# Kernel optimization log

Hardware: AMD Instinct MI355X
Metric: run time of the kernel (lower is better)

The kernel has to match this reference:

```python
import jax, jax.numpy as jnp
import numpy as np

N = 50000      # nodes
E = 800000     # edges (avg degree 16)
D = 64         # dim_inner
L = 2          # layers_mp
OUT = 2        # dim_out (fraud / not fraud)
LN_EPS = 1e-5


def setup_inputs() -> dict:
    key = jax.random.key(0)
    ks = jax.random.split(key, 12)
    rn = lambda k, shape: jax.random.normal(k, shape, dtype=jnp.float32) * 0.05
    return {
        "x": jax.random.normal(ks[0], (N, D), dtype=jnp.float32),
        "edge_attr": jax.random.normal(ks[1], (E, D), dtype=jnp.float32),
        "edge_index": jax.random.randint(ks[2], (2, E), 0, N),
        # GINEConv inner MLP: Linear(D,D) -> ReLU -> Linear(D,D), stacked over L layers
        "gine_w1": rn(ks[3], (L, D, D)), "gine_b1": jnp.zeros((L, D), jnp.float32),
        "gine_w2": rn(ks[4], (L, D, D)), "gine_b2": jnp.zeros((L, D), jnp.float32),
        # edge-update MLP: Linear(3D,D) -> ReLU -> Linear(D,D)
        "em_w1": rn(ks[5], (L, 3 * D, D)), "em_b1": jnp.zeros((L, D), jnp.float32),
        "em_w2": rn(ks[6], (L, D, D)), "em_b2": jnp.zeros((L, D), jnp.float32),
        # per-layer LayerNorm params
        "ln_g": jnp.ones((L, D), jnp.float32), "ln_b": jnp.zeros((L, D), jnp.float32),
        # post_mp head: Linear(D, OUT)
        "head_w": rn(ks[7], (D, OUT)), "head_b": jnp.zeros((OUT,), jnp.float32),
    }


def _layernorm(h, g, b):
    mu = h.mean(axis=-1, keepdims=True)
    var = h.var(axis=-1, keepdims=True)
    return (h - mu) * jax.lax.rsqrt(var + LN_EPS) * g + b


def reference(x, edge_attr, edge_index, gine_w1, gine_b1, gine_w2, gine_b2,
              em_w1, em_b1, em_w2, em_b2, ln_g, ln_b, head_w, head_b):
    src, dst = edge_index[0], edge_index[1]
    e = edge_attr
    for i in range(L):
        # GINEConv: sum_{j->i} relu(x_j + e_ji), eps=0 so (1+eps)*x_i = x_i
        msg = jax.nn.relu(x[src] + e)                         # [E, D] gather + fuse
        agg = jax.ops.segment_sum(msg, dst, num_segments=N)   # [N, D] scatter-add
        h = x + agg
        h = jax.nn.relu(h @ gine_w1[i] + gine_b1[i]) @ gine_w2[i] + gine_b2[i]
        # norm -> activation (dropout p=0 in eval)
        x = jax.nn.relu(_layernorm(h, ln_g[i], ln_b[i]))
        # edge update: e = e + emlp(cat[x_src, x_dst, e]) / 2
        cat = jnp.concatenate([x[src], x[dst], e], axis=-1)   # [E, 3D]
        e = e + (jax.nn.relu(cat @ em_w1[i] + em_b1[i]) @ em_w2[i] + em_b2[i]) * 0.5
    # post_mp head on node features
    return x @ head_w + head_b
```

## Files before the change

### kernel.cpp

```cpp
#include <hip/hip_runtime.h>
#include <hip/hip_bf16.h>

#define NN 50000
#define NE 800000
#define D 64
#define K3 (3 * D)
#define LNEPS 1e-5f
#define STR 68
#define SINB 200
#define SHB 72
#define SEB 68

typedef __attribute__((ext_vector_type(8))) short bf16x8;
typedef __attribute__((ext_vector_type(4))) float f32x4;

__device__ __forceinline__ unsigned cvt2(float lo, float hi) {
  __hip_bfloat162 h = __float22bfloat162_rn(make_float2(lo, hi));
  return *(unsigned*)&h;
}
__device__ __forceinline__ unsigned short f2bf(float f) {
  __hip_bfloat16 h = __float2bfloat16(f);
  return *(unsigned short*)&h;
}
__device__ __forceinline__ float bf2f(unsigned short s) {
  return __uint_as_float((unsigned)s << 16);
}

#define FMA4x4(v, w)                                                  \
  a0.x = fmaf(v.x, w.x, a0.x); a0.y = fmaf(v.x, w.y, a0.y);           \
  a0.z = fmaf(v.x, w.z, a0.z); a0.w = fmaf(v.x, w.w, a0.w);           \
  a1.x = fmaf(v.y, w.x, a1.x); a1.y = fmaf(v.y, w.y, a1.y);           \
  a1.z = fmaf(v.y, w.z, a1.z); a1.w = fmaf(v.y, w.w, a1.w);           \
  a2.x = fmaf(v.z, w.x, a2.x); a2.y = fmaf(v.z, w.y, a2.y);           \
  a2.z = fmaf(v.z, w.z, a2.z); a2.w = fmaf(v.z, w.w, a2.w);           \
  a3.x = fmaf(v.w, w.x, a3.x); a3.y = fmaf(v.w, w.y, a3.y);           \
  a3.z = fmaf(v.w, w.z, a3.z); a3.w = fmaf(v.w, w.w, a3.w);

#define FMA2x4(v, w)                                                  \
  a0.x = fmaf(v.x, w.x, a0.x); a0.y = fmaf(v.x, w.y, a0.y);           \
  a0.z = fmaf(v.x, w.z, a0.z); a0.w = fmaf(v.x, w.w, a0.w);           \
  a1.x = fmaf(v.y, w.x, a1.x); a1.y = fmaf(v.y, w.y, a1.y);           \
  a1.z = fmaf(v.y, w.z, a1.z); a1.w = fmaf(v.y, w.w, a1.w);

#define HSTORE_RELU(buf)                                              \
  buf[(j0+0)*STR + t0+0] = fmaxf(a0.x, 0.f);                          \
  buf[(j0+1)*STR + t0+0] = fmaxf(a0.y, 0.f);                          \
  buf[(j0+2)*STR + t0+0] = fmaxf(a0.z, 0.f);                          \
  buf[(j0+3)*STR + t0+0] = fmaxf(a0.w, 0.f);                          \
  buf[(j0+0)*STR + t0+1] = fmaxf(a1.x, 0.f);                          \
  buf[(j0+1)*STR + t0+1] = fmaxf(a1.y, 0.f);                          \
  buf[(j0+2)*STR + t0+1] = fmaxf(a1.z, 0.f);                          \
  buf[(j0+3)*STR + t0+1] = fmaxf(a1.w, 0.f);                          \
  buf[(j0+0)*STR + t0+2] = fmaxf(a2.x, 0.f);                          \
  buf[(j0+1)*STR + t0+2] = fmaxf(a2.y, 0.f);                          \
  buf[(j0+2)*STR + t0+2] = fmaxf(a2.z, 0.f);                          \
  buf[(j0+3)*STR + t0+2] = fmaxf(a2.w, 0.f);                          \
  buf[(j0+0)*STR + t0+3] = fmaxf(a3.x, 0.f);                          \
  buf[(j0+1)*STR + t0+3] = fmaxf(a3.y, 0.f);                          \
  buf[(j0+2)*STR + t0+3] = fmaxf(a3.z, 0.f);                          \
  buf[(j0+3)*STR + t0+3] = fmaxf(a3.w, 0.f);

__global__ __launch_bounds__(256) void count_kernel(
    const int* __restrict__ dst, int* __restrict__ deg) {
  int e = blockIdx.x * 256 + threadIdx.x;
  if (e < NE) atomicAdd(&deg[dst[e]], 1);
}

__global__ __launch_bounds__(1024) void scan_reduce_kernel(
    const int* __restrict__ deg, int* __restrict__ bsum) {
  __shared__ int sS[16];
  int i = blockIdx.x * 1024 + threadIdx.x;
  int v = (i < NN) ? deg[i] : 0;
#pragma unroll
  for (int o = 32; o > 0; o >>= 1) v += __shfl_down(v, o, 64);
  if ((threadIdx.x & 63) == 0) sS[threadIdx.x >> 6] = v;
  __syncthreads();
  if (threadIdx.x == 0) {
    int s = 0;
#pragma unroll
    for (int k = 0; k < 16; ++k) s += sS[k];
    bsum[blockIdx.x] = s;
  }
}

__global__ __launch_bounds__(1024) void scan_final_kernel(
    const int* __restrict__ deg, const int* __restrict__ bsum,
    int* __restrict__ off, int* __restrict__ cur) {
  __shared__ int sD[1024];
  __shared__ int sOfs;
  const int t = threadIdx.x;
  const int b = blockIdx.x;
  int i = b * 1024 + t;
  int v = (i < NN) ? deg[i] : 0;
  sD[t] = v;
  if (t == 0) {
    int o = 0;
    for (int k = 0; k < b; ++k) o += bsum[k];
    sOfs = o;
  }
  __syncthreads();
  for (int st = 1; st < 1024; st <<= 1) {
    int add = (t >= st) ? sD[t - st] : 0;
    __syncthreads();
    sD[t] += add;
    __syncthreads();
  }
  if (i < NN) {
    int excl = sOfs + sD[t] - v;
    off[i] = excl;
    cur[i] = excl;
    if (i == NN - 1) off[NN] = NE;
  }
}

__global__ __launch_bounds__(256) void fill_kernel(
    const int* __restrict__ src, const int* __restrict__ dst,
    int* __restrict__ cur, int2* __restrict__ epair, int* __restrict__ dcsr) {
  int e = blockIdx.x * 256 + threadIdx.x;
  if (e < NE) {
    int d = dst[e];
    int p = atomicAdd(&cur[d], 1);
    epair[p] = make_int2(e, src[e]);
    dcsr[p] = d;
  }
}

__global__ __launch_bounds__(256) void pack_weights_kernel(
    const float* __restrict__ w1, const float* __restrict__ w2,
    unsigned short* __restrict__ wB1, unsigned short* __restrict__ wB2) {
  int tid = blockIdx.x * 256 + threadIdx.x;
  const float* wsrc;
  unsigned short* wdst;
  int kb, j, slot;
  if (tid < 1536) {
    int nt = tid / 384, kk = (tid / 64) % 6, l = tid & 63;
    kb = kk * 32 + (l >> 4) * 8;
    j = nt * 16 + (l & 15);
    wsrc = w1; wdst = wB1; slot = tid;
  } else {
    int t = tid - 1536;
    int nt = t / 128, kk = (t / 64) & 1, l = t & 63;
    kb = kk * 32 + (l >> 4) * 8;
    j = nt * 16 + (l & 15);
    wsrc = w2; wdst = wB2; slot = t;
  }
  unsigned short b[8];
#pragma unroll
  for (int i = 0; i < 8; ++i) b[i] = f2bf(wsrc[(kb + i) * D + j]);
  uint4 v;
  v.x = (unsigned)b[0] | ((unsigned)b[1] << 16);
  v.y = (unsigned)b[2] | ((unsigned)b[3] << 16);
  v.z = (unsigned)b[4] | ((unsigned)b[5] << 16);
  v.w = (unsigned)b[6] | ((unsigned)b[7] << 16);
  *(uint4*)(wdst + (size_t)slot * 8) = v;
}

__device__ __forceinline__ void mlp_tail512(
    float* sIN, float* sH, float* sPS, float* sPQ, float* sMu, float* sRs,
    const float* __restrict__ w1, const float* __restrict__ b1,
    const float* __restrict__ w2, const float* __restrict__ b2,
    const float* __restrict__ g, const float* __restrict__ bln,
    float* __restrict__ xo, unsigned short* __restrict__ xob,
    const float* __restrict__ hw, const float* __restrict__ hb,
    float* __restrict__ outh,
    int n0, int tid) {
  __syncthreads();
  const int tj = tid & 15, tt = tid >> 4;
  const int j0 = tj * 4, t0 = tt * 2;
  float4 a0, a1;

  {
    float4 bv = *(const float4*)(b1 + j0);
    a0 = a1 = bv;
    for (int k = 0; k < D; ++k) {
      float4 w = *(const float4*)(w1 + k * D + j0);
      float2 v = *(const float2*)&sIN[k * STR + t0];
      FMA2x4(v, w)
    }
  }
  sH[(j0 + 0) * STR + t0 + 0] = fmaxf(a0.x, 0.f);
  sH[(j0 + 1) * STR + t0 + 0] = fmaxf(a0.y, 0.f);
  sH[(j0 + 2) * STR + t0 + 0] = fmaxf(a0.z, 0.f);
  sH[(j0 + 3) * STR + t0 + 0] = fmaxf(a0.w, 0.f);
  sH[(j0 + 0) * STR + t0 + 1] = fmaxf(a1.x, 0.f);
  sH[(j0 + 1) * STR + t0 + 1] = fmaxf(a1.y, 0.f);
  sH[(j0 + 2) * STR + t0 + 1] = fmaxf(a1.z, 0.f);
  sH[(j0 + 3) * STR + t0 + 1] = fmaxf(a1.w, 0.f);
  __syncthreads();

  {
    float4 bv = *(const float4*)(b2 + j0);
    a0 = a1 = bv;
    for (int k = 0; k < D; ++k) {
      float4 w = *(const float4*)(w2 + k * D + j0);
      float2 v = *(const float2*)&sH[k * STR + t0];
      FMA2x4(v, w)
    }
  }
  __syncthreads();
  *(float4*)&sH[(t0 + 0) * STR + j0] = a0;
  *(float4*)&sH[(t0 + 1) * STR + j0] = a1;
  __syncthreads();

  {
    const int t = tid & 63, p = tid >> 6;
    const float* r = &sH[t * STR + p * 8];
    float s = 0.f, q = 0.f;
#pragma unroll
    for (int i = 0; i < 8; ++i) { float v = r[i]; s += v; q = fmaf(v, v, q); }
    sPS[p * 64 + t] = s;
    sPQ[p * 64 + t] = q;
  }
  __syncthreads();
  if (tid < 64) {
    float s = 0.f, q = 0.f;
#pragma unroll
    for (int p = 0; p < 8; ++p) { s += sPS[p * 64 + tid]; q += sPQ[p * 64 + tid]; }
    float mu = s * (1.f / 64.f);
    float var = q * (1.f / 64.f) - mu * mu;
    sMu[tid] = mu;
    sRs[tid] = rsqrtf(var + LNEPS);
  }
  __syncthreads();

  {
    const int t = tid >> 3, c = (tid & 7) * 8;
    int node = n0 + t;
    if (node < NN) {
      float mu = sMu[t], rs = sRs[t];
      float4 v0 = *(const float4*)&sH[t * STR + c + 0];
      float4 v1 = *(const float4*)&sH[t * STR + c + 4];
      float4 g0v = *(const float4*)(g + c + 0);
      float4 g1v = *(const float4*)(g + c + 4);
      float4 b0v = *(const float4*)(bln + c + 0);
      float4 b1v = *(const float4*)(bln + c + 4);
      float4 r0, r1;
      r0.x = fmaxf(fmaf((v0.x - mu) * rs, g0v.x, b0v.x), 0.f);
      r0.y = fmaxf(fmaf((v0.y - mu) * rs, g0v.y, b0v.y), 0.f);
      r0.z = fmaxf(fmaf((v0.z - mu) * rs, g0v.z, b0v.z), 0.f);
      r0.w = fmaxf(fmaf((v0.w - mu) * rs, g0v.w, b0v.w), 0.f);
      r1.x = fmaxf(fmaf((v1.x - mu) * rs, g1v.x, b1v.x), 0.f);
      r1.y = fmaxf(fmaf((v1.y - mu) * rs, g1v.y, b1v.y), 0.f);
      r1.z = fmaxf(fmaf((v1.z - mu) * rs, g1v.z, b1v.z), 0.f);
      r1.w = fmaxf(fmaf((v1.w - mu) * rs, g1v.w, b1v.w), 0.f);
      if (outh) {
        float h0, h1;
        h0 = r0.x * hw[(c + 0) * 2 + 0] + r0.y * hw[(c + 1) * 2 + 0] +
             r0.z * hw[(c + 2) * 2 + 0] + r0.w * hw[(c + 3) * 2 + 0] +
             r1.x * hw[(c + 4) * 2 + 0] + r1.y * hw[(c + 5) * 2 + 0] +
             r1.z * hw[(c + 6) * 2 + 0] + r1.w * hw[(c + 7) * 2 + 0];
        h1 = r0.x * hw[(c + 0) * 2 + 1] + r0.y * hw[(c + 1) * 2 + 1] +
             r0.z * hw[(c + 2) * 2 + 1] + r0.w * hw[(c + 3) * 2 + 1] +
             r1.x * hw[(c + 4) * 2 + 1] + r1.y * hw[(c + 5) * 2 + 1] +
             r1.z * hw[(c + 6) * 2 + 1] + r1.w * hw[(c + 7) * 2 + 1];
#pragma unroll
        for (int o = 1; o < 8; o <<= 1) {
          h0 += __shfl_xor(h0, o, 64);
          h1 += __shfl_xor(h1, o, 64);
        }
        if ((tid & 7) == 0) {
          outh[node * 2 + 0] = h0 + hb[0];
          outh[node * 2 + 1] = h1 + hb[1];
        }
      } else {
        float* o = xo + (size_t)node * D + c;
        ((float4*)o)[0] = r0;
        ((float4*)o)[1] = r1;
        if (xob) {
          uint4 u;
          u.x = cvt2(r0.x, r0.y); u.y = cvt2(r0.z, r0.w);
          u.z = cvt2(r1.x, r1.y); u.w = cvt2(r1.z, r1.w);
          *(uint4*)(xob + (size_t)node * D + c) = u;
        }
      }
    }
  }
}

__global__ __launch_bounds__(512) void node_mlp_g0_kernel(
    const float* __restrict__ x, const float* __restrict__ e,
    const int2* __restrict__ epair, const int* __restrict__ off,
    const float* __restrict__ w1, const float* __restrict__ b1,
    const float* __restrict__ w2, const float* __restrict__ b2,
    const float* __restrict__ g, const float* __restrict__ bln,
    float* __restrict__ xo, unsigned short* __restrict__ xob,
    unsigned short* __restrict__ ecsr) {
  __shared__ float sIN[D * STR];
  __shared__ float sH[D * STR];
  __shared__ float sPS[512], sPQ[512], sMu[64], sRs[64];
  const int tid = threadIdx.x;
  const int n0 = blockIdx.x * 64;
  const int wv = tid >> 6, lane = tid & 63;
  for (int q = 0; q < 8; ++q) {
    int t = wv * 8 + q;
    int node = n0 + t;
    float acc = 0.f;
    if (node < NN) {
      acc = x[(size_t)node * D + lane];
      int beg = off[node], end = off[node + 1];
      int i = beg;
      for (; i + 7 < end; i += 8) {
        int2 p0 = epair[i + 0], p1 = epair[i + 1];
        int2 p2 = epair[i + 2], p3 = epair[i + 3];
        int2 p4 = epair[i + 4], p5 = epair[i + 5];
        int2 p6 = epair[i + 6], p7 = epair[i + 7];
        float x0v = x[(size_t)p0.y * D + lane], e0v = e[(size_t)p0.x * D + lane];
        float x1v = x[(size_t)p1.y * D + lane], e1v = e[(size_t)p1.x * D + lane];
        float x2v = x[(size_t)p2.y * D + lane], e2v = e[(size_t)p2.x * D + lane];
        float x3v = x[(size_t)p3.y * D + lane], e3v = e[(size_t)p3.x * D + lane];
        float x4v = x[(size_t)p4.y * D + lane], e4v = e[(size_t)p4.x * D + lane];
        float x5v = x[(size_t)p5.y * D + lane], e5v = e[(size_t)p5.x * D + lane];
        float x6v = x[(size_t)p6.y * D + lane], e6v = e[(size_t)p6.x * D + lane];
        float x7v = x[(size_t)p7.y * D + lane], e7v = e[(size_t)p7.x * D + lane];
        ecsr[(size_t)(i + 0) * D + lane] = f2bf(e0v);
        ecsr[(size_t)(i + 1) * D + lane] = f2bf(e1v);
        ecsr[(size_t)(i + 2) * D + lane] = f2bf(e2v);
        ecsr[(size_t)(i + 3) * D + lane] = f2bf(e3v);
        ecsr[(size_t)(i + 4) * D + lane] = f2bf(e4v);
        ecsr[(size_t)(i + 5) * D + lane] = f2bf(e5v);
        ecsr[(size_t)(i + 6) * D + lane] = f2bf(e6v);
        ecsr[(size_t)(i + 7) * D + lane] = f2bf(e7v);
        acc += ((fmaxf(x0v + e0v, 0.f) + fmaxf(x1v + e1v, 0.f)) +
                (fmaxf(x2v + e2v, 0.f) + fmaxf(x3v + e3v, 0.f))) +
               ((fmaxf(x4v + e4v, 0.f) + fmaxf(x5v + e5v, 0.f)) +
                (fmaxf(x6v + e6v, 0.f) + fmaxf(x7v + e7v, 0.f)));
      }
      for (; i + 3 < end; i += 4) {
        int2 p0 = epair[i + 0], p1 = epair[i + 1];
        int2 p2 = epair[i + 2], p3 = epair[i + 3];
        float x0v = x[(size_t)p0.y * D + lane], e0v = e[(size_t)p0.x * D + lane];
        float x1v = x[(size_t)p1.y * D + lane], e1v = e[(size_t)p1.x * D + lane];
        float x2v = x[(size_t)p2.y * D + lane], e2v = e[(size_t)p2.x * D + lane];
        float x3v = x[(size_t)p3.y * D + lane], e3v = e[(size_t)p3.x * D + lane];
        ecsr[(size_t)(i + 0) * D + lane] = f2bf(e0v);
        ecsr[(size_t)(i + 1) * D + lane] = f2bf(e1v);
        ecsr[(size_t)(i + 2) * D + lane] = f2bf(e2v);
        ecsr[(size_t)(i + 3) * D + lane] = f2bf(e3v);
        acc += (fmaxf(x0v + e0v, 0.f) + fmaxf(x1v + e1v, 0.f)) +
               (fmaxf(x2v + e2v, 0.f) + fmaxf(x3v + e3v, 0.f));
      }
      for (; i < end; ++i) {
        int2 pa = epair[i];
        float va = e[(size_t)pa.x * D + lane];
        ecsr[(size_t)i * D + lane] = f2bf(va);
        acc += fmaxf(x[(size_t)pa.y * D + lane] + va, 0.f);
      }
    }
    sIN[lane * STR + t] = acc;
  }
  mlp_tail512(sIN, sH, sPS, sPQ, sMu, sRs, w1, b1, w2, b2, g, bln,
              xo, xob, nullptr, nullptr, nullptr, n0, tid);
}

__global__ __launch_bounds__(512) void node_mlp_g1_kernel(
    const float* __restrict__ x, const unsigned short* __restrict__ msg,
    const int* __restrict__ off,
    const float* __restrict__ w1, const float* __restrict__ b1,
    const float* __restrict__ w2, const float* __restrict__ b2,
    const float* __restrict__ g, const float* __restrict__ bln,
    const float* __restrict__ hw, const float* __restrict__ hb,
    float* __restrict__ outh) {
  __shared__ float sIN[D * STR];
  __shared__ float sH[D * STR];
  __shared__ float sPS[512], sPQ[512], sMu[64], sRs[64];
  const int tid = threadIdx.x;
  const int n0 = blockIdx.x * 64;
  const int wv = tid >> 6, lane = tid & 63;
  for (int q = 0; q < 8; ++q) {
    int t = wv * 8 + q;
    int node = n0 + t;
    float acc = 0.f;
    if (node < NN) {
      acc = x[(size_t)node * D + lane];
      int beg = off[node], end = off[node + 1];
      const unsigned short* mr = msg + (size_t)beg * D + lane;
      int cnt = end - beg, i = 0;
      for (; i + 7 < cnt; i += 8) {
        float m0 = bf2f(mr[(size_t)(i + 0) * D]);
        float m1 = bf2f(mr[(size_t)(i + 1) * D]);
        float m2 = bf2f(mr[(size_t)(i + 2) * D]);
        float m3 = bf2f(mr[(size_t)(i + 3) * D]);
        float m4 = bf2f(mr[(size_t)(i + 4) * D]);
        float m5 = bf2f(mr[(size_t)(i + 5) * D]);
        float m6 = bf2f(mr[(size_t)(i + 6) * D]);
        float m7 = bf2f(mr[(size_t)(i + 7) * D]);
        acc += ((m0 + m1) + (m2 + m3)) + ((m4 + m5) + (m6 + m7));
      }
      for (; i < cnt; ++i) acc += bf2f(mr[(size_t)i * D]);
    }
    sIN[lane * STR + t] = acc;
  }
  mlp_tail512(sIN, sH, sPS, sPQ, sMu, sRs, w1, b1, w2, b2, g, bln,
              nullptr, nullptr, hw, hb, outh, n0, tid);
}

__global__ __launch_bounds__(256) void edge_mfma_csr_kernel(
    const unsigned short* __restrict__ x1b, const unsigned short* __restrict__ ecsr,
    const int2* __restrict__ epair, const int* __restrict__ dcsr,
    const unsigned short* __restrict__ wB1, const float* __restrict__ b1,
    const unsigned short* __restrict__ wB2, const float* __restrict__ b2,
    unsigned short* __restrict__ msg) {
  __shared__ unsigned short sIN[64 * SINB];
  __shared__ unsigned short sH[64 * SHB];

  const int tid = threadIdx.x;
  const int e0 = blockIdx.x * 64;
  const int lane = tid & 63;
  const int mt = tid >> 6;
  const int hl = lane >> 4;
  const int ll = lane & 15;

  {
    const int t = tid & 63, p = tid >> 6;
    int slot = e0 + t;
    int sN = epair[slot].y;
    int dN = dcsr[slot];
    const uint4* xs = (const uint4*)(x1b + (size_t)sN * D + p * 16);
    const uint4* xd = (const uint4*)(x1b + (size_t)dN * D + p * 16);
    const uint4* ec = (const uint4*)(ecsr + (size_t)slot * D + p * 16);
    uint4* r0 = (uint4*)(sIN + t * SINB + p * 16);
    uint4* r1 = (uint4*)(sIN + t * SINB + 64 + p * 16);
    uint4* r2 = (uint4*)(sIN + t * SINB + 128 + p * 16);
    uint4 a0v = xs[0], a1v = xs[1];
    uint4 b0v = xd[0], b1v = xd[1];
    uint4 c0v = ec[0], c1v = ec[1];
    r0[0] = a0v; r0[1] = a1v;
    r1[0] = b0v; r1[1] = b1v;
    r2[0] = c0v; r2[1] = c1v;
  }
  __syncthreads();

  f32x4 acc[4];
#pragma unroll
  for (int nt = 0; nt < 4; ++nt) {
    float b = b1[nt * 16 + ll];
    acc[nt].x = b; acc[nt].y = b; acc[nt].z = b; acc[nt].w = b;
  }
  {
    const unsigned short* aBase = sIN + (mt * 16 + ll) * SINB + hl * 8;
#pragma unroll
    for (int kk = 0; kk < 6; ++kk) {
      bf16x8 af = *(const bf16x8*)(aBase + kk * 32);
#pragma unroll
      for (int nt = 0; nt < 4; ++nt) {
        bf16x8 bf = *(const bf16x8*)(wB1 + ((size_t)(nt * 6 + kk) * 64 + lane) * 8);
        acc[nt] = __builtin_amdgcn_mfma_f32_16x16x32_bf16(af, bf, acc[nt], 0, 0, 0);
      }
    }
  }
#pragma unroll
  for (int nt = 0; nt < 4; ++nt)
#pragma unroll
    for (int r = 0; r < 4; ++r)
      sH[(mt * 16 + hl * 4 + r) * SHB + nt * 16 + ll] = f2bf(fmaxf(acc[nt][r], 0.f));
  __syncthreads();

  f32x4 acc2[4];
#pragma unroll
  for (int nt = 0; nt < 4; ++nt) {
    float b = b2[nt * 16 + ll];
    acc2[nt].x = b; acc2[nt].y = b; acc2[nt].z = b; acc2[nt].w = b;
  }
  {
    const unsigned short* hBase = sH + (mt * 16 + ll) * SHB + hl * 8;
#pragma unroll
    for (int kk = 0; kk < 2; ++kk) {
      bf16x8 af = *(const bf16x8*)(hBase + kk * 32);
#pragma unroll
      for (int nt = 0; nt < 4; ++nt) {
        bf16x8 bf = *(const bf16x8*)(wB2 + ((size_t)(nt * 2 + kk) * 64 + lane) * 8);
        acc2[nt] = __builtin_amdgcn_mfma_f32_16x16x32_bf16(af, bf, acc2[nt], 0, 0, 0);
      }
    }
  }

#pragma unroll
  for (int r = 0; r < 4; ++r) {
    int t = mt * 16 + hl * 4 + r;
    int slot = e0 + t;
    const unsigned short* xr = sIN + t * SINB;
    const unsigned short* er = sIN + t * SINB + 128;
    unsigned short* mr = msg + (size_t)slot * D;
#pragma unroll
    for (int nt = 0; nt < 4; ++nt) {
      int j = nt * 16 + ll;
      float xf = bf2f(xr[j]);
      float ef = bf2f(er[j]);
      mr[j] = f2bf(fmaxf(xf + fmaf(0.5f, acc2[nt][r], ef), 0.f));
    }
  }
}

__global__ __launch_bounds__(256) void scatter_kernel(
    const float* __restrict__ x, const float* __restrict__ e,
    const int* __restrict__ src, const int* __restrict__ dst,
    float* __restrict__ agg) {
  int tid = blockIdx.x * blockDim.x + threadIdx.x;
  if (tid >= NE * 16) return;
  int eid = tid >> 4, q = tid & 15;
  int s = src[eid], d = dst[eid];
  float4 xv = ((const float4*)(x + (size_t)s * D))[q];
  float4 ev = ((const float4*)(e + (size_t)eid * D))[q];
  float* a = agg + (size_t)d * D + q * 4;
  atomicAdd(a + 0, fmaxf(xv.x + ev.x, 0.f));
  atomicAdd(a + 1, fmaxf(xv.y + ev.y, 0.f));
  atomicAdd(a + 2, fmaxf(xv.z + ev.z, 0.f));
  atomicAdd(a + 3, fmaxf(xv.w + ev.w, 0.f));
}

__device__ __forceinline__ void mlp_tail256(
    float* sIN, float* sH, float* sPS, float* sPQ, float* sMu, float* sRs,
    const float* __restrict__ w1, const float* __restrict__ b1,
    const float* __restrict__ w2, const float* __restrict__ b2,
    const float* __restrict__ g, const float* __restrict__ bln,
    float* __restrict__ xo, int n0, int tid) {
  __syncthreads();
  const int tj = tid & 15, tt = tid >> 4;
  const int j0 = tj * 4, t0 = tt * 4;
  float4 a0, a1, a2, a3;
  {
    float4 bv = *(const float4*)(b1 + j0);
    a0 = a1 = a2 = a3 = bv;
    for (int k = 0; k < D; ++k) {
      float4 w = *(const float4*)(w1 + k * D + j0);
      float4 v = *(const float4*)&sIN[k * STR + t0];
      FMA4x4(v, w)
    }
  }
  HSTORE_RELU(sH)
  __syncthreads();
  {
    float4 bv = *(const float4*)(b2 + j0);
    a0 = a1 = a2 = a3 = bv;
    for (int k = 0; k < D; ++k) {
      float4 w = *(const float4*)(w2 + k * D + j0);
      float4 v = *(const float4*)&sH[k * STR + t0];
      FMA4x4(v, w)
    }
  }
  __syncthreads();
  *(float4*)&sH[(t0 + 0) * STR + j0] = a0;
  *(float4*)&sH[(t0 + 1) * STR + j0] = a1;
  *(float4*)&sH[(t0 + 2) * STR + j0] = a2;
  *(float4*)&sH[(t0 + 3) * STR + j0] = a3;
  __syncthreads();
  {
    const int t = tid & 63, p = tid >> 6;
    const float* r = &sH[t * STR + p * 16];
    float s = 0.f, q = 0.f;
#pragma unroll
    for (int i = 0; i < 16; ++i) { float v = r[i]; s += v; q = fmaf(v, v, q); }
    sPS[p * 64 + t] = s;
    sPQ[p * 64 + t] = q;
  }
  __syncthreads();
  if (tid < 64) {
    float s = sPS[tid] + sPS[64 + tid] + sPS[128 + tid] + sPS[192 + tid];
    float q = sPQ[tid] + sPQ[64 + tid] + sPQ[128 + tid] + sPQ[192 + tid];
    float mu = s * (1.f / 64.f);
    float var = q * (1.f / 64.f) - mu * mu;
    sMu[tid] = mu;
    sRs[tid] = rsqrtf(var + LNEPS);
  }
  __syncthreads();
  {
    const int t = tid >> 2, c = (tid & 3) * 16;
    int node = n0 + t;
    if (node < NN) {
      float mu = sMu[t], rs = sRs[t];
      float* o = xo + (size_t)node * D + c;
#pragma unroll
      for (int i = 0; i < 4; ++i) {
        float4 v = *(const float4*)&sH[t * STR + c + i * 4];
        float4 gv = *(const float4*)(g + c + i * 4);
        float4 bv = *(const float4*)(bln + c + i * 4);
        float4 r;
        r.x = fmaxf(fmaf((v.x - mu) * rs, gv.x, bv.x), 0.f);
        r.y = fmaxf(fmaf((v.y - mu) * rs, gv.y, bv.y), 0.f);
        r.z = fmaxf(fmaf((v.z - mu) * rs, gv.z, bv.z), 0.f);
        r.w = fmaxf(fmaf((v.w - mu) * rs, gv.w, bv.w), 0.f);
        ((float4*)o)[i] = r;
      }
    }
  }
}

__global__ __launch_bounds__(256) void node_mlp_kernel(
    const float* __restrict__ x, const float* __restrict__ agg,
    const float* __restrict__ w1, const float* __restrict__ b1,
    const float* __restrict__ w2, const float* __restrict__ b2,
    const float* __restrict__ g, const float* __restrict__ bln,
    float* __restrict__ xo) {
  __shared__ float sIN[D * STR];
  __shared__ float sH[D * STR];
  __shared__ float sPS[256], sPQ[256], sMu[64], sRs[64];
  const int tid = threadIdx.x;
  const int n0 = blockIdx.x * 64;
  {
    const int t = tid & 63, p = tid >> 6;
    int node = n0 + t;
    int cn = node < NN ? node : 0;
    const float* xr = x + (size_t)cn * D + p * 16;
    const float* ar = agg + (size_t)cn * D + p * 16;
#pragma unroll
    for (int i = 0; i < 4; ++i) {
      float4 xv = ((const float4*)xr)[i];
      float4 av = ((const float4*)ar)[i];
      int k = p * 16 + i * 4;
      sIN[(k + 0) * STR + t] = xv.x + av.x;
      sIN[(k + 1) * STR + t] = xv.y + av.y;
      sIN[(k + 2) * STR + t] = xv.z + av.z;
      sIN[(k + 3) * STR + t] = xv.w + av.w;
    }
  }
  mlp_tail256(sIN, sH, sPS, sPQ, sMu, sRs, w1, b1, w2, b2, g, bln, xo, n0, tid);
}

__global__ __launch_bounds__(256) void edge_mfma_atomic_kernel(
    const float* __restrict__ x, const float* __restrict__ e,
    const int* __restrict__ src, const int* __restrict__ dst,
    const unsigned short* __restrict__ wB1, const float* __restrict__ b1,
    const unsigned short* __restrict__ wB2, const float* __restrict__ b2,
    float* __restrict__ agg) {
  __shared__ unsigned short sIN[64 * SINB];
  __shared__ unsigned short sH[64 * SHB];
  __shared__ float sE[64 * SEB];
  const int tid = threadIdx.x;
  const int e0 = blockIdx.x * 64;
  const int lane = tid & 63;
  const int mt = tid >> 6;
  const int hl = lane >> 4;
  const int ll = lane & 15;
  {
    const int t = tid & 63, p = tid >> 6;
    int eid = e0 + t;
    int sN = src[eid], dN = dst[eid];
    const float* g0 = x + (size_t)sN * D + p * 16;
    const float* g1 = x + (size_t)dN * D + p * 16;
    const float* g2 = e + (size_t)eid * D + p * 16;
    unsigned short* row = sIN + t * SINB + p * 16;
#pragma unroll
    for (int i = 0; i < 4; ++i) {
      float4 v0 = ((const float4*)g0)[i];
      float4 v1 = ((const float4*)g1)[i];
      float4 v2 = ((const float4*)g2)[i];
      uint2 u;
      u.x = cvt2(v0.x, v0.y); u.y = cvt2(v0.z, v0.w);
      *(uint2*)(row + i * 4) = u;
      u.x = cvt2(v1.x, v1.y); u.y = cvt2(v1.z, v1.w);
      *(uint2*)(row + 64 + i * 4) = u;
      u.x = cvt2(v2.x, v2.y); u.y = cvt2(v2.z, v2.w);
      *(uint2*)(row + 128 + i * 4) = u;
      *(float4*)&sE[t * SEB + p * 16 + i * 4] = v2;
    }
  }
  __syncthreads();
  f32x4 acc[4];
#pragma unroll
  for (int nt = 0; nt < 4; ++nt) {
    float b = b1[nt * 16 + ll];
    acc[nt].x = b; acc[nt].y = b; acc[nt].z = b; acc[nt].w = b;
  }
  {
    const unsigned short* aBase = sIN + (mt * 16 + ll) * SINB + hl * 8;
#pragma unroll
    for (int kk = 0; kk < 6; ++kk) {
      bf16x8 af = *(const bf16x8*)(aBase + kk * 32);
#pragma unroll
      for (int nt = 0; nt < 4; ++nt) {
        bf16x8 bf = *(const bf16x8*)(wB1 + ((size_t)(nt * 6 + kk) * 64 + lane) * 8);
        acc[nt] = __builtin_amdgcn_mfma_f32_16x16x32_bf16(af, bf, acc[nt], 0, 0, 0);
      }
    }
  }
#pragma unroll
  for (int nt = 0; nt < 4; ++nt)
#pragma unroll
    for (int r = 0; r < 4; ++r)
      sH[(mt * 16 + hl * 4 + r) * SHB + nt * 16 + ll] = f2bf(fmaxf(acc[nt][r], 0.f));
  __syncthreads();
  f32x4 acc2[4];
#pragma unroll
  for (int nt = 0; nt < 4; ++nt) {
    float b = b2[nt * 16 + ll];
    acc2[nt].x = b; acc2[nt].y = b; acc2[nt].z = b; acc2[nt].w = b;
  }
  {
    const unsigned short* hBase = sH + (mt * 16 + ll) * SHB + hl * 8;
#pragma unroll
    for (int kk = 0; kk < 2; ++kk) {
      bf16x8 af = *(const bf16x8*)(hBase + kk * 32);
#pragma unroll
      for (int nt = 0; nt < 4; ++nt) {
        bf16x8 bf = *(const bf16x8*)(wB2 + ((size_t)(nt * 2 + kk) * 64 + lane) * 8);
        acc2[nt] = __builtin_amdgcn_mfma_f32_16x16x32_bf16(af, bf, acc2[nt], 0, 0, 0);
      }
    }
  }
#pragma unroll
  for (int r = 0; r < 4; ++r) {
    int t = mt * 16 + hl * 4 + r;
    int eid = e0 + t;
    int sN = src[eid], dN = dst[eid];
    const float* xr = x + (size_t)sN * D;
    const float* er = &sE[t * SEB];
    float* ar = agg + (size_t)dN * D;
#pragma unroll
    for (int nt = 0; nt < 4; ++nt) {
      int j = nt * 16 + ll;
      atomicAdd(ar + j, fmaxf(xr[j] + fmaf(0.5f, acc2[nt][r], er[j]), 0.f));
    }
  }
}

__global__ __launch_bounds__(256) void head_kernel(
    const float* __restrict__ x, const float* __restrict__ w,
    const float* __restrict__ b, float* __restrict__ out) {
  int nid = blockIdx.x * blockDim.x + threadIdx.x;
  if (nid >= NN) return;
  const float* xr = x + (size_t)nid * D;
  float a0 = b[0], a1 = b[1];
  for (int k = 0; k < D; ++k) {
    float v = xr[k];
    a0 = fmaf(v, w[k * 2 + 0], a0);
    a1 = fmaf(v, w[k * 2 + 1], a1);
  }
  out[nid * 2 + 0] = a0;
  out[nid * 2 + 1] = a1;
}

extern "C" void kernel_launch(void* const* d_in, const int* in_sizes, int n_in,
                              void* d_out, int out_size, void* d_ws, size_t ws_size,
                              hipStream_t stream) {
  const float* x0  = (const float*)d_in[0];
  const float* e0  = (const float*)d_in[1];
  const int*   ei  = (const int*)d_in[2];
  const float* gw1 = (const float*)d_in[3];
  const float* gb1 = (const float*)d_in[4];
  const float* gw2 = (const float*)d_in[5];
  const float* gb2 = (const float*)d_in[6];
  const float* ew1 = (const float*)d_in[7];
  const float* eb1 = (const float*)d_in[8];
  const float* ew2 = (const float*)d_in[9];
  const float* eb2 = (const float*)d_in[10];
  const float* lng = (const float*)d_in[11];
  const float* lnb = (const float*)d_in[12];
  const float* hw  = (const float*)d_in[13];
  const float* hb  = (const float*)d_in[14];
  float* out = (float*)d_out;

  char* ws = (char*)d_ws;
  const size_t SZ_X     = (size_t)NN * D * 4;
  const size_t OFF_X1   = 0;
  const size_t OFF_WB1  = OFF_X1 + SZ_X;
  const size_t OFF_WB2  = OFF_WB1 + 24576;
  const size_t OFF_DEG  = OFF_WB2 + 8192;
  const size_t OFF_OFFS = OFF_DEG + 200704;
  const size_t OFF_CUR  = OFF_OFFS + 200704;
  const size_t OFF_BSUM = OFF_CUR + 200704;
  const size_t OFF_EPAIR= OFF_BSUM + 512;
  const size_t OFF_DCSR = OFF_EPAIR + (size_t)NE * 8;
  const size_t OFF_X1B  = OFF_DCSR + (size_t)NE * 4;
  const size_t OFF_ECSR = OFF_X1B + (size_t)NN * D * 2;
  const size_t OFF_MSG  = OFF_ECSR + (size_t)NE * D * 2;
  const size_t NEED_A   = OFF_MSG + (size_t)NE * D * 2;

  float* x1   = (float*)(ws + OFF_X1);
  unsigned short* wB1 = (unsigned short*)(ws + OFF_WB1);
  unsigned short* wB2 = (unsigned short*)(ws + OFF_WB2);
  int* deg  = (int*)(ws + OFF_DEG);
  int* offs = (int*)(ws + OFF_OFFS);
  int* cur  = (int*)(ws + OFF_CUR);
  int* bsum = (int*)(ws + OFF_BSUM);
  int2* epair = (int2*)(ws + OFF_EPAIR);
  int* dcsr = (int*)(ws + OFF_DCSR);
  unsigned short* x1b  = (unsigned short*)(ws + OFF_X1B);
  unsigned short* ecsr = (unsigned short*)(ws + OFF_ECSR);
  unsigned short* msg  = (unsigned short*)(ws + OFF_MSG);

  const int* src = ei;
  const int* dst = ei + NE;

  const int nodeBlocks = (NN + 63) / 64;
  const int edgeBlocks = NE / 64;
  const int scanBlocks = (NN + 1023) / 1024;

  pack_weights_kernel<<<8, 256, 0, stream>>>(ew1, ew2, wB1, wB2);

  if (ws_size >= NEED_A) {
    hipMemsetAsync(deg, 0, (size_t)NN * 4, stream);
    count_kernel<<<(NE + 255) / 256, 256, 0, stream>>>(dst, deg);
    scan_reduce_kernel<<<scanBlocks, 1024, 0, stream>>>(deg, bsum);
    scan_final_kernel<<<scanBlocks, 1024, 0, stream>>>(deg, bsum, offs, cur);
    fill_kernel<<<(NE + 255) / 256, 256, 0, stream>>>(src, dst, cur, epair, dcsr);

    node_mlp_g0_kernel<<<nodeBlocks, 512, 0, stream>>>(
        x0, e0, epair, offs, gw1, gb1, gw2, gb2, lng, lnb, x1, x1b, ecsr);

    edge_mfma_csr_kernel<<<edgeBlocks, 256, 0, stream>>>(
        x1b, ecsr, epair, dcsr, wB1, eb1, wB2, eb2, msg);

    node_mlp_g1_kernel<<<nodeBlocks, 512, 0, stream>>>(
        x1, msg, offs, gw1 + D * D, gb1 + D, gw2 + D * D, gb2 + D,
        lng + D, lnb + D, hw, hb, out);
  } else {
    float* agg = (float*)(ws + OFF_EPAIR);
    float* x2  = (float*)(ws + OFF_EPAIR + SZ_X);
    hipMemsetAsync(agg, 0, SZ_X, stream);
    scatter_kernel<<<(NE * 16 + 255) / 256, 256, 0, stream>>>(x0, e0, src, dst, agg);
    node_mlp_kernel<<<nodeBlocks, 256, 0, stream>>>(
        x0, agg, gw1, gb1, gw2, gb2, lng, lnb, x1);
    hipMemsetAsync(agg, 0, SZ_X, stream);
    edge_mfma_atomic_kernel<<<edgeBlocks, 256, 0, stream>>>(
        x1, e0, src, dst, wB1, eb1, wB2, eb2, agg);
    node_mlp_kernel<<<nodeBlocks, 256, 0, stream>>>(
        x1, agg, gw1 + D * D, gb1 + D, gw2 + D * D, gb2 + D, lng + D, lnb + D, x2);
    head_kernel<<<(NN + 255) / 256, 256, 0, stream>>>(x2, hw, hb, out);
  }
}
```

Measured before the change: 406.4 us.

## Permute edge features into CSR order with a separate coalesced kernel

fill_kernel now records each edge's CSR position, and a new permute_e_kernel reads edge_attr rows contiguously in float4 chunks and scatters bf16 rows into CSR order. node_mlp_g0 then reads the bf16 ecsr stream sequentially instead of gathering fp32 e rows by edge id and writing ecsr itself. The goal is to replace random 256-byte row gathers with coalesced reads and bf16 reads in the aggregation. In exchange it adds a kernel launch, a pos array and an extra read pass over ecsr. The g0 and g1 aggregation loops also drop from 8-way to 4-way unrolling.

```diff
diff --git a/kernel.cpp b/kernel.cpp
--- a/kernel.cpp
+++ b/kernel.cpp
@@ -115,14 +115,35 @@
 
 __global__ __launch_bounds__(256) void fill_kernel(
     const int* __restrict__ src, const int* __restrict__ dst,
-    int* __restrict__ cur, int2* __restrict__ epair, int* __restrict__ dcsr) {
+    int* __restrict__ cur, int2* __restrict__ epair,
+    int* __restrict__ dcsr, int* __restrict__ pos) {
   int e = blockIdx.x * 256 + threadIdx.x;
   if (e < NE) {
     int d = dst[e];
     int p = atomicAdd(&cur[d], 1);
     epair[p] = make_int2(e, src[e]);
     dcsr[p] = d;
-  }
+    pos[e] = p;
+  }
+}
+
+__global__ __launch_bounds__(256) void permute_e_kernel(
+    const float* __restrict__ e, const int* __restrict__ pos,
+    unsigned short* __restrict__ ecsr) {
+  int tid = blockIdx.x * 256 + threadIdx.x;
+  int eid = tid >> 2, q = tid & 3;
+  if (eid >= NE) return;
+  int p = pos[eid];
+  const float4* srcp = (const float4*)(e + (size_t)eid * D + q * 16);
+  float4 v0 = srcp[0], v1 = srcp[1], v2 = srcp[2], v3 = srcp[3];
+  uint4 u0, u1;
+  u0.x = cvt2(v0.x, v0.y); u0.y = cvt2(v0.z, v0.w);
+  u0.z = cvt2(v1.x, v1.y); u0.w = cvt2(v1.z, v1.w);
+  u1.x = cvt2(v2.x, v2.y); u1.y = cvt2(v2.z, v2.w);
+  u1.z = cvt2(v3.x, v3.y); u1.w = cvt2(v3.z, v3.w);
+  uint4* dstp = (uint4*)(ecsr + (size_t)p * D + q * 16);
+  dstp[0] = u0;
+  dstp[1] = u1;
 }
 
 __global__ __launch_bounds__(256) void pack_weights_kernel(
@@ -278,13 +299,12 @@
 }
 
 __global__ __launch_bounds__(512) void node_mlp_g0_kernel(
-    const float* __restrict__ x, const float* __restrict__ e,
+    const float* __restrict__ x, const unsigned short* __restrict__ ecsr,
     const int2* __restrict__ epair, const int* __restrict__ off,
     const float* __restrict__ w1, const float* __restrict__ b1,
     const float* __restrict__ w2, const float* __restrict__ b2,
     const float* __restrict__ g, const float* __restrict__ bln,
-    float* __restrict__ xo, unsigned short* __restrict__ xob,
-    unsigned short* __restrict__ ecsr) {
+    float* __restrict__ xo, unsigned short* __restrict__ xob) {
   __shared__ float sIN[D * STR];
   __shared__ float sH[D * STR];
   __shared__ float sPS[512], sPQ[512], sMu[64], sRs[64];
@@ -298,52 +318,21 @@
     if (node < NN) {
       acc = x[(size_t)node * D + lane];
       int beg = off[node], end = off[node + 1];
-      int i = beg;
-      for (; i + 7 < end; i += 8) {
-        int2 p0 = epair[i + 0], p1 = epair[i + 1];
-        int2 p2 = epair[i + 2], p3 = epair[i + 3];
-        int2 p4 = epair[i + 4], p5 = epair[i + 5];
-        int2 p6 = epair[i + 6], p7 = epair[i + 7];
-        float x0v = x[(size_t)p0.y * D + lane], e0v = e[(size_t)p0.x * D + lane];
-        float x1v = x[(size_t)p1.y * D + lane], e1v = e[(size_t)p1.x * D + lane];
-        float x2v = x[(size_t)p2.y * D + lane], e2v = e[(size_t)p2.x * D + lane];
-        float x3v = x[(size_t)p3.y * D + lane], e3v = e[(size_t)p3.x * D + lane];
-        float x4v = x[(size_t)p4.y * D + lane], e4v = e[(size_t)p4.x * D + lane];
-        float x5v = x[(size_t)p5.y * D + lane], e5v = e[(size_t)p5.x * D + lane];
-        float x6v = x[(size_t)p6.y * D + lane], e6v = e[(size_t)p6.x * D + lane];
-        float x7v = x[(size_t)p7.y * D + lane], e7v = e[(size_t)p7.x * D + lane];
-        ecsr[(size_t)(i + 0) * D + lane] = f2bf(e0v);
-        ecsr[(size_t)(i + 1) * D + lane] = f2bf(e1v);
-        ecsr[(size_t)(i + 2) * D + lane] = f2bf(e2v);
-        ecsr[(size_t)(i + 3) * D + lane] = f2bf(e3v);
-        ecsr[(size_t)(i + 4) * D + lane] = f2bf(e4v);
-        ecsr[(size_t)(i + 5) * D + lane] = f2bf(e5v);
-        ecsr[(size_t)(i + 6) * D + lane] = f2bf(e6v);
-        ecsr[(size_t)(i + 7) * D + lane] = f2bf(e7v);
-        acc += ((fmaxf(x0v + e0v, 0.f) + fmaxf(x1v + e1v, 0.f)) +
-                (fmaxf(x2v + e2v, 0.f) + fmaxf(x3v + e3v, 0.f))) +
-               ((fmaxf(x4v + e4v, 0.f) + fmaxf(x5v + e5v, 0.f)) +
-                (fmaxf(x6v + e6v, 0.f) + fmaxf(x7v + e7v, 0.f)));
+      const unsigned short* er = ecsr + (size_t)beg * D + lane;
+      int cnt = end - beg, i = 0;
+      for (; i + 3 < cnt; i += 4) {
+        int s0 = epair[beg + i + 0].y, s1 = epair[beg + i + 1].y;
+        int s2 = epair[beg + i + 2].y, s3 = epair[beg + i + 3].y;
+        float xa = x[(size_t)s0 * D + lane], ea = bf2f(er[(size_t)(i + 0) * D]);
+        float xb = x[(size_t)s1 * D + lane], eb = bf2f(er[(size_t)(i + 1) * D]);
+        float xc = x[(size_t)s2 * D + lane], ec = bf2f(er[(size_t)(i + 2) * D]);
+        float xd = x[(size_t)s3 * D + lane], ed = bf2f(er[(size_t)(i + 3) * D]);
+        acc += (fmaxf(xa + ea, 0.f) + fmaxf(xb + eb, 0.f)) +
+               (fmaxf(xc + ec, 0.f) + fmaxf(xd + ed, 0.f));
       }
-      for (; i + 3 < end; i += 4) {
-        int2 p0 = epair[i + 0], p1 = epair[i + 1];
-        int2 p2 = epair[i + 2], p3 = epair[i + 3];
-        float x0v = x[(size_t)p0.y * D + lane], e0v = e[(size_t)p0.x * D + lane];
-        float x1v = x[(size_t)p1.y * D + lane], e1v = e[(size_t)p1.x * D + lane];
-        float x2v = x[(size_t)p2.y * D + lane], e2v = e[(size_t)p2.x * D + lane];
-        float x3v = x[(size_t)p3.y * D + lane], e3v = e[(size_t)p3.x * D + lane];
-        ecsr[(size_t)(i + 0) * D + lane] = f2bf(e0v);
-        ecsr[(size_t)(i + 1) * D + lane] = f2bf(e1v);
-        ecsr[(size_t)(i + 2) * D + lane] = f2bf(e2v);
-        ecsr[(size_t)(i + 3) * D + lane] = f2bf(e3v);
-        acc += (fmaxf(x0v + e0v, 0.f) + fmaxf(x1v + e1v, 0.f)) +
-               (fmaxf(x2v + e2v, 0.f) + fmaxf(x3v + e3v, 0.f));
-      }
-      for (; i < end; ++i) {
-        int2 pa = epair[i];
-        float va = e[(size_t)pa.x * D + lane];
-        ecsr[(size_t)i * D + lane] = f2bf(va);
-        acc += fmaxf(x[(size_t)pa.y * D + lane] + va, 0.f);
+      for (; i < cnt; ++i) {
+        int s0 = epair[beg + i].y;
+        acc += fmaxf(x[(size_t)s0 * D + lane] + bf2f(er[(size_t)i * D]), 0.f);
       }
     }
     sIN[lane * STR + t] = acc;
@@ -375,16 +364,12 @@
       int beg = off[node], end = off[node + 1];
       const unsigned short* mr = msg + (size_t)beg * D + lane;
       int cnt = end - beg, i = 0;
-      for (; i + 7 < cnt; i += 8) {
+      for (; i + 3 < cnt; i += 4) {
         float m0 = bf2f(mr[(size_t)(i + 0) * D]);
         float m1 = bf2f(mr[(size_t)(i + 1) * D]);
         float m2 = bf2f(mr[(size_t)(i + 2) * D]);
         float m3 = bf2f(mr[(size_t)(i + 3) * D]);
-        float m4 = bf2f(mr[(size_t)(i + 4) * D]);
-        float m5 = bf2f(mr[(size_t)(i + 5) * D]);
-        float m6 = bf2f(mr[(size_t)(i + 6) * D]);
-        float m7 = bf2f(mr[(size_t)(i + 7) * D]);
-        acc += ((m0 + m1) + (m2 + m3)) + ((m4 + m5) + (m6 + m7));
+        acc += (m0 + m1) + (m2 + m3);
       }
       for (; i < cnt; ++i) acc += bf2f(mr[(size_t)i * D]);
     }
@@ -760,7 +745,8 @@
   const size_t OFF_BSUM = OFF_CUR + 200704;
   const size_t OFF_EPAIR= OFF_BSUM + 512;
   const size_t OFF_DCSR = OFF_EPAIR + (size_t)NE * 8;
-  const size_t OFF_X1B  = OFF_DCSR + (size_t)NE * 4;
+  const size_t OFF_POS  = OFF_DCSR + (size_t)NE * 4;
+  const size_t OFF_X1B  = OFF_POS + (size_t)NE * 4;
   const size_t OFF_ECSR = OFF_X1B + (size_t)NN * D * 2;
   const size_t OFF_MSG  = OFF_ECSR + (size_t)NE * D * 2;
   const size_t NEED_A   = OFF_MSG + (size_t)NE * D * 2;
@@ -774,6 +760,7 @@
   int* bsum = (int*)(ws + OFF_BSUM);
   int2* epair = (int2*)(ws + OFF_EPAIR);
   int* dcsr = (int*)(ws + OFF_DCSR);
+  int* pos  = (int*)(ws + OFF_POS);
   unsigned short* x1b  = (unsigned short*)(ws + OFF_X1B);
   unsigned short* ecsr = (unsigned short*)(ws + OFF_ECSR);
   unsigned short* msg  = (unsigned short*)(ws + OFF_MSG);
@@ -792,10 +779,12 @@
     count_kernel<<<(NE + 255) / 256, 256, 0, stream>>>(dst, deg);
     scan_reduce_kernel<<<scanBlocks, 1024, 0, stream>>>(deg, bsum);
     scan_final_kernel<<<scanBlocks, 1024, 0, stream>>>(deg, bsum, offs, cur);
-    fill_kernel<<<(NE + 255) / 256, 256, 0, stream>>>(src, dst, cur, epair, dcsr);
+    fill_kernel<<<(NE + 255) / 256, 256, 0, stream>>>(src, dst, cur, epair, dcsr, pos);
+
+    permute_e_kernel<<<(NE * 4 + 255) / 256, 256, 0, stream>>>(e0, pos, ecsr);
 
     node_mlp_g0_kernel<<<nodeBlocks, 512, 0, stream>>>(
-        x0, e0, epair, offs, gw1, gb1, gw2, gb2, lng, lnb, x1, x1b, ecsr);
+        x0, ecsr, epair, offs, gw1, gb1, gw2, gb2, lng, lnb, x1, x1b);
 
     edge_mfma_csr_kernel<<<edgeBlocks, 256, 0, stream>>>(
         x1b, ecsr, epair, dcsr, wB1, eb1, wB2, eb2, msg);
```

Result: faster. 393.2 us (-3.2%).
